# Kernel optimization log

Measured on AMD Instinct MI355X. Metric: run time of the kernel, lower is better.

The kernel has to match this reference:

```python
import jax, jax.numpy as jnp
import numpy as np

B, D, N = 2, 256, 8192   # batch, in_channels, sequence length
CI = 128                 # inter_channels
BN_EPS = 1e-5


def conv1x1(w, b, x):
    # w: (Cout, Cin), b: (Cout,), x: (B, Cin, N) -> (B, Cout, N)
    return jnp.einsum('oc,bcn->bon', w, x) + b[None, :, None]


def maxpool2(x):
    # MaxPool1d(kernel_size=2): (B, C, N) -> (B, C, N//2)
    b, c, n = x.shape
    return x.reshape(b, c, n // 2, 2).max(axis=-1)


def setup_inputs() -> dict:
    key = jax.random.key(0)
    ks = jax.random.split(key, 11)
    s_in = 1.0 / np.sqrt(D)
    s_ci = 1.0 / np.sqrt(CI)
    return {
        'f': jax.random.normal(ks[0], (B, D, N), dtype=jnp.float32),
        'g_w': jax.random.uniform(ks[1], (CI, D), jnp.float32, -s_in, s_in),
        'g_b': jax.random.uniform(ks[2], (CI,), jnp.float32, -s_in, s_in),
        'theta_w': jax.random.uniform(ks[3], (CI, D), jnp.float32, -s_in, s_in),
        'theta_b': jax.random.uniform(ks[4], (CI,), jnp.float32, -s_in, s_in),
        'phi_w': jax.random.uniform(ks[5], (CI, D), jnp.float32, -s_in, s_in),
        'phi_b': jax.random.uniform(ks[6], (CI,), jnp.float32, -s_in, s_in),
        'W_w': jax.random.uniform(ks[7], (D, CI), jnp.float32, -s_ci, s_ci),
        'W_b': jax.random.uniform(ks[8], (D,), jnp.float32, -s_ci, s_ci),
        'bn_gamma': jax.random.normal(ks[9], (D,), dtype=jnp.float32) * 0.1,
        'bn_beta': jax.random.normal(ks[10], (D,), dtype=jnp.float32) * 0.1,
    }


def reference(f, g_w, g_b, theta_w, theta_b, phi_w, phi_b, W_w, W_b, bn_gamma, bn_beta):
    # projections (1x1 convs); g and phi are sub-sampled by maxpool(2)
    g_f = maxpool2(conv1x1(g_w, g_b, f))          # (B, CI, N/2)
    theta_f = conv1x1(theta_w, theta_b, f)        # (B, CI, N)
    phi_f = maxpool2(conv1x1(phi_w, phi_b, f))    # (B, CI, N/2)

    # affinity: theta^T @ phi, softmax over keys (no scale, as in source)
    A = jnp.einsum('bcn,bcm->bnm', theta_f, phi_f)     # (B, N, N/2)
    A = jax.nn.softmax(A, axis=-1)
    y = jnp.einsum('bnm,bcm->bcn', A, g_f)             # (B, CI, N)

    # W: 1x1 conv + BatchNorm1d (training-mode batch stats), residual
    Wy = conv1x1(W_w, W_b, y)                          # (B, D, N)
    mean = Wy.mean(axis=(0, 2), keepdims=True)
    var = Wy.var(axis=(0, 2), keepdims=True)           # biased, like torch BN
    Wy = (Wy - mean) * jax.lax.rsqrt(var + BN_EPS)
    Wy = Wy * bn_gamma[None, :, None] + bn_beta[None, :, None]
    return Wy + f
```

## Files before the change

kernel.cpp:

```cpp
#include <hip/hip_runtime.h>
#include <hip/hip_bf16.h>
#include <math.h>

#define B_ 2
#define D_ 256
#define N_ 8192
#define CI_ 128
#define M_ 4096
#define BN_EPS_ 1e-5f
#define LOG2E_ 1.4426950408889634f

#define GLOBAL_AS __attribute__((address_space(1)))
#define LDS_AS __attribute__((address_space(3)))

#define OFF_WALL 0
#define OFF_THT  65536
#define OFF_PHT  (OFF_THT + 1048576)
#define OFF_GT   (OFF_PHT + 524288)
#define OFF_YP   (OFF_GT  + 524288)
#define OFF_ML   (OFF_YP  + 4194304)
#define OFF_MEAN (OFF_ML + 131072)
#define OFF_RSTD (OFF_MEAN + 256)

typedef __attribute__((ext_vector_type(8))) short bfrag;
typedef __attribute__((ext_vector_type(4))) float f4v;
typedef __attribute__((ext_vector_type(16))) float f16v;
typedef __attribute__((ext_vector_type(4))) short s4v;
typedef __attribute__((ext_vector_type(4))) unsigned u4v;

__device__ inline unsigned short bf16rne(float x) {
    unsigned u = __float_as_uint(x);
    u += 0x7fff + ((u >> 16) & 1);
    return (unsigned short)(u >> 16);
}

__device__ inline float exp2fast(float x) {
    float r;
    asm("v_exp_f32 %0, %1" : "=v"(r) : "v"(x));
    return r;
}

__global__ __launch_bounds__(256) void wconv_kernel(
    const float* __restrict__ gw, const float* __restrict__ tw, const float* __restrict__ pw,
    const float* __restrict__ Ww, short* __restrict__ wall)
{
    int idx = blockIdx.x * 256 + threadIdx.x;
    int which = idx >> 15;
    int rem = idx & 32767;
    const float* src = (which == 0) ? gw : (which == 1) ? tw : (which == 2) ? pw : Ww;
    float v = src[rem];
    if (which == 1) v *= LOG2E_;
    wall[idx] = (short)bf16rne(v);
}

__global__ __launch_bounds__(256, 2) void proj_kernel(
    const float* __restrict__ f, const short* __restrict__ wall,
    const float* __restrict__ tb, const float* __restrict__ gb, const float* __restrict__ pb,
    short* __restrict__ th_t, short* __restrict__ g_t, short* __restrict__ ph_t)
{
    __shared__ short sF[32 * 72];

    const int tid = threadIdx.x;
    const int wave = tid >> 6, lane = tid & 63;
    const int lq = lane & 15, quad = lane >> 4;
    const int b = blockIdx.y;
    const int n0 = blockIdx.x * 32;

    const float* fb = f + (size_t)b * D_ * N_;

    f4v acc[6][2];
#pragma unroll
    for (int ct = 0; ct < 6; ct++)
#pragma unroll
        for (int nf = 0; nf < 2; nf++) acc[ct][nf] = (f4v){0.f, 0.f, 0.f, 0.f};

    const int sn = tid & 31;
    const int sgrp = tid >> 5;

    for (int kc = 0; kc < D_; kc += 64) {
        __syncthreads();
#pragma unroll
        for (int jj = 0; jj < 4; jj++) {
            int dd = kc + sgrp * 8 + 2 * jj;
            float v0 = fb[(size_t)dd * N_ + n0 + sn];
            float v1 = fb[(size_t)(dd + 1) * N_ + n0 + sn];
            unsigned pk = (unsigned)bf16rne(v0) | ((unsigned)bf16rne(v1) << 16);
            *(unsigned*)&sF[sn * 72 + sgrp * 8 + 2 * jj] = pk;
        }
        __syncthreads();

        bfrag afr[6][2], bfr[2][2];
#pragma unroll
        for (int ks = 0; ks < 2; ks++) {
#pragma unroll
            for (int nf = 0; nf < 2; nf++)
                bfr[nf][ks] = *(const bfrag*)&sF[(nf * 16 + lq) * 72 + ks * 32 + quad * 8];
#pragma unroll
            for (int ct = 0; ct < 6; ct++)
                afr[ct][ks] = *(const bfrag*)&wall[(wave * 96 + ct * 16 + lq) * 256 + kc + ks * 32 + quad * 8];
        }
#pragma unroll
        for (int ks = 0; ks < 2; ks++)
#pragma unroll
            for (int ct = 0; ct < 6; ct++) {
                acc[ct][0] = __builtin_amdgcn_mfma_f32_16x16x32_bf16(afr[ct][ks], bfr[0][ks], acc[ct][0], 0, 0, 0);
                acc[ct][1] = __builtin_amdgcn_mfma_f32_16x16x32_bf16(afr[ct][ks], bfr[1][ks], acc[ct][1], 0, 0, 0);
            }
    }

#pragma unroll
    for (int ct = 0; ct < 6; ct++) {
        const int cf = wave * 6 + ct;
#pragma unroll
        for (int nf = 0; nf < 2; nf++) {
            f4v v = acc[ct][nf];
            const int n = n0 + nf * 16 + lq;
            if (cf < 8) {
                const int cb = cf * 16 + quad * 4;
                float pl[4];
#pragma unroll
                for (int r = 0; r < 4; r++) {
                    float o = __shfl_xor(v[r], 1);
                    pl[r] = fmaxf(v[r], o) + gb[cb + r];
                }
                if (!(lq & 1)) {
                    const int m = n >> 1;
#pragma unroll
                    for (int r = 0; r < 4; r++)
                        g_t[((size_t)b * CI_ + cb + r) * M_ + m] = (short)bf16rne(pl[r]);
                }
            } else if (cf < 16) {
                const int cb = (cf - 8) * 16 + quad * 4;
                s4v o;
#pragma unroll
                for (int r = 0; r < 4; r++) o[r] = (short)bf16rne(v[r] + tb[cb + r] * LOG2E_);
                *(s4v*)&th_t[((size_t)b * N_ + n) * CI_ + cb] = o;
            } else {
                const int cb = (cf - 16) * 16 + quad * 4;
                float pl[4];
#pragma unroll
                for (int r = 0; r < 4; r++) {
                    float o = __shfl_xor(v[r], 1);
                    pl[r] = fmaxf(v[r], o) + pb[cb + r];
                }
                if (!(lq & 1)) {
                    const int m = n >> 1;
                    s4v o;
#pragma unroll
                    for (int r = 0; r < 4; r++) o[r] = (short)bf16rne(pl[r]);
                    *(s4v*)&ph_t[((size_t)b * M_ + m) * CI_ + cb] = o;
                }
            }
        }
    }
}

__global__ __launch_bounds__(256, 2) void attn_kernel(
    const short* __restrict__ th_p, const short* __restrict__ ph_p,
    const short* __restrict__ g_p, short* __restrict__ yp, float* __restrict__ ml)
{
    __shared__ short sPh[2][64 * 128];
    __shared__ short sG [2][128 * 72];

    const int tid = threadIdx.x;
    const int wave = tid >> 6, lane = tid & 63;
    const int l = lane & 31, h = lane >> 5;

    const int bid = blockIdx.x;
    const int b = bid & 1;
    const int split = (bid >> 1) & 3;
    const int q0 = (bid >> 3) * 128;
    const int qg = q0 + wave * 32 + l;

    const short* thr = th_p + ((size_t)b * N_ + qg) * CI_;
    bfrag tf[8];
#pragma unroll
    for (int s = 0; s < 8; s++)
        tf[s] = *(const bfrag*)&thr[s * 16 + h * 8];

    f16v yacc[4];
#pragma unroll
    for (int ct = 0; ct < 4; ct++)
#pragma unroll
        for (int r = 0; r < 16; r++) yacc[ct][r] = 0.f;
    float mI = -INFINITY, lI = 0.f;

    const short* phg = ph_p + (size_t)b * M_ * CI_;
    const short* gg  = g_p + (size_t)b * CI_ * M_;

    const int k0 = split * 1024;
    const int xm = l & 15;

    const int prow = (lane >> 4);
    const int pslot = lane & 15;

    const int i0 = (wave < 2) ? wave * 5 : 10 + (wave - 2) * 4;
    const int nIss = (wave < 2) ? 5 : 4;
    int gsrc[5];
#pragma unroll
    for (int p = 0; p < 5; p++) {
        const int t = (i0 + p) * 64 + lane;
        gsrc[p] = (t / 9) * M_ + (t % 9) * 8;
    }

#define STAGE_DMA(BUF, KC)                                                                  \
    do {                                                                                    \
        _Pragma("unroll")                                                                   \
        for (int p = 0; p < 4; p++) {                                                       \
            const int rp = wave * 16 + p * 4 + prow;                     \
            const int cg = pslot ^ (p * 4 + prow);                   \
            __builtin_amdgcn_global_load_lds(                                               \
                (const GLOBAL_AS void*)(phg + (size_t)((KC) + rp) * 128 + cg * 8),          \
                (LDS_AS void*)(&sPh[BUF][(wave * 16 + p * 4) * 128]), 16, 0, 0);            \
        }                                                                                   \
        _Pragma("unroll")                                                                   \
        for (int p = 0; p < 5; p++) {                                                       \
            if (p < nIss)                                                                   \
                __builtin_amdgcn_global_load_lds(                                           \
                    (const GLOBAL_AS void*)(gg + gsrc[p] + (KC)),                           \
                    (LDS_AS void*)(&sG[BUF][(i0 + p) * 512]), 16, 0, 0);                    \
        }                                                                                   \
    } while (0)

    STAGE_DMA(0, k0);

    int cur = 0;
    for (int kc = k0; kc < k0 + 1024; kc += 64) {
        __syncthreads();
        const bool nxt = (kc + 64 < k0 + 1024);
        if (nxt) {
            STAGE_DMA(cur ^ 1, kc + 64);
            __builtin_amdgcn_sched_barrier(0);
        }

        f16v sv[2];
        __builtin_amdgcn_s_setprio(1);
#pragma unroll
        for (int kt = 0; kt < 2; kt++) {
            f16v a;
#pragma unroll
            for (int r = 0; r < 16; r++) a[r] = 0.f;
#pragma unroll
            for (int s = 0; s < 8; s++) {
                bfrag pa = *(const bfrag*)&sPh[cur][(kt * 32 + l) * 128 + (((s << 1) | h) ^ xm) * 8];
                a = __builtin_amdgcn_mfma_f32_32x32x16_bf16(pa, tf[s], a, 0, 0, 0);
            }
            sv[kt] = a;
        }
        __builtin_amdgcn_s_setprio(0);

        float mx = fmaxf(sv[0][0], sv[1][0]);
#pragma unroll
        for (int r = 1; r < 16; r++) mx = fmaxf(mx, fmaxf(sv[0][r], sv[1][r]));
        mx = fmaxf(mx, __shfl_xor(mx, 32));

        if (__any(mx > mI + 8.f)) {
            float mnew = fmaxf(mI, mx);
            float al = exp2fast(mI - mnew);
            lI *= al;
#pragma unroll
            for (int ct = 0; ct < 4; ct++)
#pragma unroll
                for (int r = 0; r < 16; r++) yacc[ct][r] *= al;
            mI = mnew;
        }

        float ps = 0.f;
        unsigned pw[16];
#pragma unroll
        for (int kt = 0; kt < 2; kt++)
#pragma unroll
            for (int i = 0; i < 8; i++) {
                const int r = 2 * i;
                float p0 = exp2fast(sv[kt][r] - mI);
                float p1 = exp2fast(sv[kt][r + 1] - mI);
                ps += p0 + p1;
                unsigned pk;
                asm("v_cvt_pk_bf16_f32 %0, %1, %2" : "=v"(pk) : "v"(p0), "v"(p1));
                pw[kt * 8 + (i >> 1) * 2 + (i & 1)] = pk;
            }
        ps += __shfl_xor(ps, 32);
        lI += ps;

        bfrag pf[4];
#pragma unroll
        for (int s = 0; s < 4; s++) {
            const int kt = s >> 1;
            const int iA = kt * 8 + ((2 * s) & 3) * 2;
            const int iB = kt * 8 + ((2 * s + 1) & 3) * 2;
            unsigned A0 = pw[iA], A1 = pw[iA + 1];
            unsigned B0 = pw[iB], B1 = pw[iB + 1];
            unsigned O0 = h ? B0 : A0;
            unsigned O1 = h ? B1 : A1;
            unsigned Xs0 = h ? A0 : B0;
            unsigned Xs1 = h ? A1 : B1;
            unsigned X0 = (unsigned)__shfl_xor((int)Xs0, 32);
            unsigned X1 = (unsigned)__shfl_xor((int)Xs1, 32);
            u4v t;
            t.x = h ? X0 : O0;
            t.y = h ? X1 : O1;
            t.z = h ? O0 : X0;
            t.w = h ? O1 : X1;
            pf[s] = __builtin_bit_cast(bfrag, t);
        }

        __builtin_amdgcn_s_setprio(1);
#pragma unroll
        for (int ct = 0; ct < 4; ct++)
#pragma unroll
            for (int s = 0; s < 4; s++) {
                bfrag ga = *(const bfrag*)&sG[cur][(ct * 32 + l) * 72 + s * 16 + h * 8];
                yacc[ct] = __builtin_amdgcn_mfma_f32_32x32x16_bf16(ga, pf[s], yacc[ct], 0, 0, 0);
            }
        __builtin_amdgcn_s_setprio(0);

        cur ^= 1;
    }
#undef STAGE_DMA

    short* yb = yp + (((size_t)split * B_ + b) * N_) * CI_;
#pragma unroll
    for (int ct = 0; ct < 4; ct++)
#pragma unroll
        for (int rq = 0; rq < 4; rq++) {
            const int c0 = ct * 32 + 8 * rq + 4 * h;
            s4v o;
#pragma unroll
            for (int j = 0; j < 4; j++) o[j] = (short)bf16rne(yacc[ct][rq * 4 + j]);
            *(s4v*)&yb[(size_t)qg * CI_ + c0] = o;
        }
    if (h == 0) {
        float* mlb = ml + ((split * B_ + b) * 2) * N_;
        mlb[qg] = mI;
        mlb[N_ + qg] = lI;
    }
}

__global__ __launch_bounds__(256) void wy_merge_kernel(
    const short* __restrict__ yp, const float* __restrict__ ml,
    const short* __restrict__ wall2, const float* __restrict__ Wb,
    float* __restrict__ out)
{
    const int tid = threadIdx.x;
    const int wave = tid >> 6, lane = tid & 63;
    const int l = lane & 31, h = lane >> 5;
    const int b = blockIdx.y;
    const int n = blockIdx.x * 32 + l;

    float m[4], lv[4];
#pragma unroll
    for (int sp = 0; sp < 4; sp++) {
        const float* mlb = ml + ((sp * B_ + b) * 2) * N_;
        m[sp] = mlb[n];
        lv[sp] = mlb[N_ + n];
    }
    float mmax = fmaxf(fmaxf(m[0], m[1]), fmaxf(m[2], m[3]));
    float e[4], den = 0.f;
#pragma unroll
    for (int sp = 0; sp < 4; sp++) { e[sp] = exp2fast(m[sp] - mmax); den += lv[sp] * e[sp]; }
    float inv = 1.0f / den;
#pragma unroll
    for (int sp = 0; sp < 4; sp++) e[sp] *= inv;

    bfrag by[8];
#pragma unroll
    for (int s = 0; s < 8; s++) {
        float a[8];
#pragma unroll
        for (int j = 0; j < 8; j++) a[j] = 0.f;
#pragma unroll
        for (int sp = 0; sp < 4; sp++) {
            bfrag yv = *(const bfrag*)&yp[(((size_t)sp * B_ + b) * N_ + n) * CI_ + s * 16 + h * 8];
            u4v u = __builtin_bit_cast(u4v, yv);
#pragma unroll
            for (int p = 0; p < 4; p++) {
                a[2 * p]     = fmaf(e[sp], __uint_as_float(u[p] << 16), a[2 * p]);
                a[2 * p + 1] = fmaf(e[sp], __uint_as_float(u[p] & 0xffff0000u), a[2 * p + 1]);
            }
        }
        u4v pk;
#pragma unroll
        for (int p = 0; p < 4; p++) {
            unsigned r;
            asm("v_cvt_pk_bf16_f32 %0, %1, %2" : "=v"(r) : "v"(a[2 * p]), "v"(a[2 * p + 1]));
            pk[p] = r;
        }
        by[s] = __builtin_bit_cast(bfrag, pk);
    }

    f16v acc[2];
#pragma unroll
    for (int rt = 0; rt < 2; rt++)
#pragma unroll
        for (int r = 0; r < 16; r++) acc[rt][r] = 0.f;

#pragma unroll
    for (int s = 0; s < 8; s++)
#pragma unroll
        for (int rt = 0; rt < 2; rt++) {
            bfrag aw = *(const bfrag*)&wall2[((wave * 2 + rt) * 32 + l) * 128 + s * 16 + h * 8];
            acc[rt] = __builtin_amdgcn_mfma_f32_32x32x16_bf16(aw, by[s], acc[rt], 0, 0, 0);
        }

#pragma unroll
    for (int rt = 0; rt < 2; rt++)
#pragma unroll
        for (int r = 0; r < 16; r++) {
            const int d = (wave * 2 + rt) * 32 + (r & 3) + 8 * (r >> 2) + 4 * h;
            out[((size_t)b * D_ + d) * N_ + n] = acc[rt][r] + Wb[d];
        }
}

__global__ __launch_bounds__(256) void stats_kernel(
    const float* __restrict__ wy, float* __restrict__ mean, float* __restrict__ rstd)
{
    __shared__ float ssum[256], ssq[256];
    int d = blockIdx.x;
    int tid = threadIdx.x;
    float s = 0.f, sq = 0.f;
    for (int b = 0; b < B_; b++) {
        const float4* p = (const float4*)(wy + (size_t)b * D_ * N_ + (size_t)d * N_);
        for (int i = tid; i < N_ / 4; i += 256) {
            float4 v = p[i];
            s += v.x + v.y + v.z + v.w;
            sq = fmaf(v.x, v.x, sq);
            sq = fmaf(v.y, v.y, sq);
            sq = fmaf(v.z, v.z, sq);
            sq = fmaf(v.w, v.w, sq);
        }
    }
    ssum[tid] = s; ssq[tid] = sq;
    __syncthreads();
    for (int st = 128; st > 0; st >>= 1) {
        if (tid < st) { ssum[tid] += ssum[tid + st]; ssq[tid] += ssq[tid + st]; }
        __syncthreads();
    }
    if (tid == 0) {
        float inv = 1.0f / (float)(B_ * N_);
        float mn = ssum[0] * inv;
        float var = ssq[0] * inv - mn * mn;
        mean[d] = mn;
        rstd[d] = rsqrtf(var + BN_EPS_);
    }
}

__global__ __launch_bounds__(256) void bn_res_kernel(
    float* __restrict__ out, const float* __restrict__ f,
    const float* __restrict__ mean, const float* __restrict__ rstd,
    const float* __restrict__ gamma, const float* __restrict__ beta)
{
    int i = blockIdx.x * 256 + threadIdx.x;
    size_t e = (size_t)i * 4;
    int d = (int)((e >> 13) & 255);
    float4 wy = ((const float4*)out)[i];
    float4 ff = ((const float4*)f)[i];
    float sc = rstd[d] * gamma[d];
    float mn = mean[d];
    float bt = beta[d];
    float4 r;
    r.x = (wy.x - mn) * sc + bt + ff.x;
    r.y = (wy.y - mn) * sc + bt + ff.y;
    r.z = (wy.z - mn) * sc + bt + ff.z;
    r.w = (wy.w - mn) * sc + bt + ff.w;
    ((float4*)out)[i] = r;
}

extern "C" void kernel_launch(void* const* d_in, const int* in_sizes, int n_in,
                              void* d_out, int out_size, void* d_ws, size_t ws_size,
                              hipStream_t stream)
{
    const float* f   = (const float*)d_in[0];
    const float* g_w = (const float*)d_in[1];
    const float* g_b = (const float*)d_in[2];
    const float* t_w = (const float*)d_in[3];
    const float* t_b = (const float*)d_in[4];
    const float* p_w = (const float*)d_in[5];
    const float* p_b = (const float*)d_in[6];
    const float* W_w = (const float*)d_in[7];
    const float* W_b = (const float*)d_in[8];
    const float* gam = (const float*)d_in[9];
    const float* bet = (const float*)d_in[10];
    float* out = (float*)d_out;
    float* ws = (float*)d_ws;

    short* wall  = (short*)(ws + OFF_WALL);
    short* wall2 = wall + 3 * 32768;
    short* th_t = (short*)(ws + OFF_THT);
    short* ph_t = (short*)(ws + OFF_PHT);
    short* g_t  = (short*)(ws + OFF_GT);
    short* ypart = (short*)(ws + OFF_YP);
    float* mlp = ws + OFF_ML;
    float* mnp = ws + OFF_MEAN;
    float* rsp = ws + OFF_RSTD;

    wconv_kernel<<<512, 256, 0, stream>>>(g_w, t_w, p_w, W_w, wall);
    proj_kernel<<<dim3(N_ / 32, B_), 256, 0, stream>>>(f, wall, t_b, g_b, p_b,
                                                       th_t, g_t, ph_t);
    attn_kernel<<<512, 256, 0, stream>>>(th_t, ph_t, g_t, ypart, mlp);
    wy_merge_kernel<<<dim3(N_ / 32, B_), 256, 0, stream>>>(ypart, mlp, wall2, W_b, out);
    stats_kernel<<<D_, 256, 0, stream>>>(out, mnp, rsp);
    bn_res_kernel<<<(B_ * D_ * N_ / 4) / 256, 256, 0, stream>>>(out, f, mnp, rsp, gam, bet);
}
```

Baseline: 180.0 us.

## Single-buffer phi tile, raise occupancy, and add 8-way key split

The phi LDS tile goes from double- to single-buffered. Its next-chunk load is now issued after a mid-iteration barrier, once the S=QK MFMAs have consumed the current tile. Launch bounds rise to 3 blocks per CU, and with a large enough workspace the key dimension is split 8 ways (1024 blocks), templating the merge kernel on the split count. The max reduction becomes a tree and the exp/pack loop is fused with the cross-half shuffle. Together these aim for more occupancy and parallelism, at the cost of an extra barrier per iteration, more partial-output traffic, and possible register spilling at 3 blocks/CU.

```diff
diff --git a/kernel.cpp b/kernel.cpp
--- a/kernel.cpp
+++ b/kernel.cpp
@@ -18,9 +18,6 @@
 #define OFF_PHT  (OFF_THT + 1048576)
 #define OFF_GT   (OFF_PHT + 524288)
 #define OFF_YP   (OFF_GT  + 524288)
-#define OFF_ML   (OFF_YP  + 4194304)
-#define OFF_MEAN (OFF_ML + 131072)
-#define OFF_RSTD (OFF_MEAN + 256)
 
 typedef __attribute__((ext_vector_type(8))) short bfrag;
 typedef __attribute__((ext_vector_type(4))) float f4v;
@@ -155,11 +152,13 @@
     }
 }
 
-__global__ __launch_bounds__(256, 2) void attn_kernel(
+template<int NS>
+__global__ __launch_bounds__(256, 3) void attn_kernel(
     const short* __restrict__ th_p, const short* __restrict__ ph_p,
     const short* __restrict__ g_p, short* __restrict__ yp, float* __restrict__ ml)
 {
-    __shared__ short sPh[2][64 * 128];
+    constexpr int SK = M_ / NS;
+    __shared__ short sPh[64 * 128];
     __shared__ short sG [2][128 * 72];
 
     const int tid = threadIdx.x;
@@ -167,9 +166,10 @@
     const int l = lane & 31, h = lane >> 5;
 
     const int bid = blockIdx.x;
-    const int b = bid & 1;
-    const int split = (bid >> 1) & 3;
-    const int q0 = (bid >> 3) * 128;
+    const int pair = bid & (2 * NS - 1);
+    const int b = pair & 1;
+    const int split = pair >> 1;
+    const int q0 = (bid / (2 * NS)) * 128;
     const int qg = q0 + wave * 32 + l;
 
     const short* thr = th_p + ((size_t)b * N_ + qg) * CI_;
@@ -188,7 +188,7 @@
     const short* phg = ph_p + (size_t)b * M_ * CI_;
     const short* gg  = g_p + (size_t)b * CI_ * M_;
 
-    const int k0 = split * 1024;
+    const int k0 = split * SK;
     const int xm = l & 15;
 
     const int prow = (lane >> 4);
@@ -203,7 +203,7 @@
         gsrc[p] = (t / 9) * M_ + (t % 9) * 8;
     }
 
-#define STAGE_DMA(BUF, KC)                                                                  \
+#define STAGE_PHI(KC)                                                                       \
     do {                                                                                    \
         _Pragma("unroll")                                                                   \
         for (int p = 0; p < 4; p++) {                                                       \
@@ -211,8 +211,11 @@
             const int cg = pslot ^ (p * 4 + prow);                   \
             __builtin_amdgcn_global_load_lds(                                               \
                 (const GLOBAL_AS void*)(phg + (size_t)((KC) + rp) * 128 + cg * 8),          \
-                (LDS_AS void*)(&sPh[BUF][(wave * 16 + p * 4) * 128]), 16, 0, 0);            \
+                (LDS_AS void*)(&sPh[(wave * 16 + p * 4) * 128]), 16, 0, 0);                 \
         }                                                                                   \
+    } while (0)
+#define STAGE_G(BUF, KC)                                                                    \
+    do {                                                                                    \
         _Pragma("unroll")                                                                   \
         for (int p = 0; p < 5; p++) {                                                       \
             if (p < nIss)                                                                   \
@@ -222,14 +225,15 @@
         }                                                                                   \
     } while (0)
 
-    STAGE_DMA(0, k0);
+    STAGE_PHI(k0);
+    STAGE_G(0, k0);
 
     int cur = 0;
-    for (int kc = k0; kc < k0 + 1024; kc += 64) {
+    for (int kc = k0; kc < k0 + SK; kc += 64) {
         __syncthreads();
-        const bool nxt = (kc + 64 < k0 + 1024);
+        const bool nxt = (kc + 64 < k0 + SK);
         if (nxt) {
-            STAGE_DMA(cur ^ 1, kc + 64);
+            STAGE_G(cur ^ 1, kc + 64);
             __builtin_amdgcn_sched_barrier(0);
         }
 
@@ -242,17 +246,31 @@
             for (int r = 0; r < 16; r++) a[r] = 0.f;
 #pragma unroll
             for (int s = 0; s < 8; s++) {
-                bfrag pa = *(const bfrag*)&sPh[cur][(kt * 32 + l) * 128 + (((s << 1) | h) ^ xm) * 8];
+                bfrag pa = *(const bfrag*)&sPh[(kt * 32 + l) * 128 + (((s << 1) | h) ^ xm) * 8];
                 a = __builtin_amdgcn_mfma_f32_32x32x16_bf16(pa, tf[s], a, 0, 0, 0);
             }
             sv[kt] = a;
         }
         __builtin_amdgcn_s_setprio(0);
 
-        float mx = fmaxf(sv[0][0], sv[1][0]);
-#pragma unroll
-        for (int r = 1; r < 16; r++) mx = fmaxf(mx, fmaxf(sv[0][r], sv[1][r]));
-        mx = fmaxf(mx, __shfl_xor(mx, 32));
+        __builtin_amdgcn_sched_barrier(0);
+        __builtin_amdgcn_s_barrier();
+        if (nxt) {
+            STAGE_PHI(kc + 64);
+            __builtin_amdgcn_sched_barrier(0);
+        }
+
+        float mx;
+        {
+            float t[16];
+#pragma unroll
+            for (int r = 0; r < 16; r++) t[r] = fmaxf(sv[0][r], sv[1][r]);
+#pragma unroll
+            for (int st = 8; st > 0; st >>= 1)
+#pragma unroll
+                for (int r = 0; r < st; r++) t[r] = fmaxf(t[r], t[r + st]);
+            mx = fmaxf(t[0], __shfl_xor(t[0], 32));
+        }
 
         if (__any(mx > mI + 8.f)) {
             float mnew = fmaxf(mI, mx);
@@ -266,34 +284,24 @@
         }
 
         float ps = 0.f;
-        unsigned pw[16];
-#pragma unroll
-        for (int kt = 0; kt < 2; kt++)
-#pragma unroll
-            for (int i = 0; i < 8; i++) {
-                const int r = 2 * i;
-                float p0 = exp2fast(sv[kt][r] - mI);
-                float p1 = exp2fast(sv[kt][r + 1] - mI);
-                ps += p0 + p1;
-                unsigned pk;
-                asm("v_cvt_pk_bf16_f32 %0, %1, %2" : "=v"(pk) : "v"(p0), "v"(p1));
-                pw[kt * 8 + (i >> 1) * 2 + (i & 1)] = pk;
-            }
-        ps += __shfl_xor(ps, 32);
-        lI += ps;
-
         bfrag pf[4];
 #pragma unroll
         for (int s = 0; s < 4; s++) {
             const int kt = s >> 1;
-            const int iA = kt * 8 + ((2 * s) & 3) * 2;
-            const int iB = kt * 8 + ((2 * s + 1) & 3) * 2;
-            unsigned A0 = pw[iA], A1 = pw[iA + 1];
-            unsigned B0 = pw[iB], B1 = pw[iB + 1];
-            unsigned O0 = h ? B0 : A0;
-            unsigned O1 = h ? B1 : A1;
-            unsigned Xs0 = h ? A0 : B0;
-            unsigned Xs1 = h ? A1 : B1;
+            const int rb = (s & 1) * 8;
+            float p[8];
+#pragma unroll
+            for (int j = 0; j < 8; j++) p[j] = exp2fast(sv[kt][rb + j] - mI);
+            ps += ((p[0] + p[1]) + (p[2] + p[3])) + ((p[4] + p[5]) + (p[6] + p[7]));
+            unsigned w0, w1, w2, w3;
+            asm("v_cvt_pk_bf16_f32 %0, %1, %2" : "=v"(w0) : "v"(p[0]), "v"(p[1]));
+            asm("v_cvt_pk_bf16_f32 %0, %1, %2" : "=v"(w1) : "v"(p[2]), "v"(p[3]));
+            asm("v_cvt_pk_bf16_f32 %0, %1, %2" : "=v"(w2) : "v"(p[4]), "v"(p[5]));
+            asm("v_cvt_pk_bf16_f32 %0, %1, %2" : "=v"(w3) : "v"(p[6]), "v"(p[7]));
+            unsigned O0 = h ? w2 : w0;
+            unsigned O1 = h ? w3 : w1;
+            unsigned Xs0 = h ? w0 : w2;
+            unsigned Xs1 = h ? w1 : w3;
             unsigned X0 = (unsigned)__shfl_xor((int)Xs0, 32);
             unsigned X1 = (unsigned)__shfl_xor((int)Xs1, 32);
             u4v t;
@@ -303,6 +311,8 @@
             t.w = h ? O1 : X1;
             pf[s] = __builtin_bit_cast(bfrag, t);
         }
+        ps += __shfl_xor(ps, 32);
+        lI += ps;
 
         __builtin_amdgcn_s_setprio(1);
 #pragma unroll
@@ -316,7 +326,8 @@
 
         cur ^= 1;
     }
-#undef STAGE_DMA
+#undef STAGE_PHI
+#undef STAGE_G
 
     short* yb = yp + (((size_t)split * B_ + b) * N_) * CI_;
 #pragma unroll
@@ -336,6 +347,7 @@
     }
 }
 
+template<int NS>
 __global__ __launch_bounds__(256) void wy_merge_kernel(
     const short* __restrict__ yp, const float* __restrict__ ml,
     const short* __restrict__ wall2, const float* __restrict__ Wb,
@@ -347,20 +359,22 @@
     const int b = blockIdx.y;
     const int n = blockIdx.x * 32 + l;
 
-    float m[4], lv[4];
-#pragma unroll
-    for (int sp = 0; sp < 4; sp++) {
+    float m[NS], lv[NS];
+#pragma unroll
+    for (int sp = 0; sp < NS; sp++) {
         const float* mlb = ml + ((sp * B_ + b) * 2) * N_;
         m[sp] = mlb[n];
         lv[sp] = mlb[N_ + n];
     }
-    float mmax = fmaxf(fmaxf(m[0], m[1]), fmaxf(m[2], m[3]));
-    float e[4], den = 0.f;
-#pragma unroll
-    for (int sp = 0; sp < 4; sp++) { e[sp] = exp2fast(m[sp] - mmax); den += lv[sp] * e[sp]; }
+    float mmax = m[0];
+#pragma unroll
+    for (int sp = 1; sp < NS; sp++) mmax = fmaxf(mmax, m[sp]);
+    float e[NS], den = 0.f;
+#pragma unroll
+    for (int sp = 0; sp < NS; sp++) { e[sp] = exp2fast(m[sp] - mmax); den += lv[sp] * e[sp]; }
     float inv = 1.0f / den;
 #pragma unroll
-    for (int sp = 0; sp < 4; sp++) e[sp] *= inv;
+    for (int sp = 0; sp < NS; sp++) e[sp] *= inv;
 
     bfrag by[8];
 #pragma unroll
@@ -369,7 +383,7 @@
 #pragma unroll
         for (int j = 0; j < 8; j++) a[j] = 0.f;
 #pragma unroll
-        for (int sp = 0; sp < 4; sp++) {
+        for (int sp = 0; sp < NS; sp++) {
             bfrag yv = *(const bfrag*)&yp[(((size_t)sp * B_ + b) * N_ + n) * CI_ + s * 16 + h * 8];
             u4v u = __builtin_bit_cast(u4v, yv);
 #pragma unroll
@@ -483,21 +497,29 @@
     float* out = (float*)d_out;
     float* ws = (float*)d_ws;
 
+    const size_t need8 = ((size_t)OFF_YP + 8u * 1048576u + 8u * 32768u + 512u) * 4u;
+    const int ns = (ws_size >= need8) ? 8 : 4;
+
     short* wall  = (short*)(ws + OFF_WALL);
     short* wall2 = wall + 3 * 32768;
     short* th_t = (short*)(ws + OFF_THT);
     short* ph_t = (short*)(ws + OFF_PHT);
     short* g_t  = (short*)(ws + OFF_GT);
     short* ypart = (short*)(ws + OFF_YP);
-    float* mlp = ws + OFF_ML;
-    float* mnp = ws + OFF_MEAN;
-    float* rsp = ws + OFF_RSTD;
+    float* mlp = ws + OFF_YP + (size_t)ns * 1048576u;
+    float* mnp = mlp + (size_t)ns * 32768u;
+    float* rsp = mnp + 256;
 
     wconv_kernel<<<512, 256, 0, stream>>>(g_w, t_w, p_w, W_w, wall);
     proj_kernel<<<dim3(N_ / 32, B_), 256, 0, stream>>>(f, wall, t_b, g_b, p_b,
                                                        th_t, g_t, ph_t);
-    attn_kernel<<<512, 256, 0, stream>>>(th_t, ph_t, g_t, ypart, mlp);
-    wy_merge_kernel<<<dim3(N_ / 32, B_), 256, 0, stream>>>(ypart, mlp, wall2, W_b, out);
+    if (ns == 8) {
+        attn_kernel<8><<<1024, 256, 0, stream>>>(th_t, ph_t, g_t, ypart, mlp);
+        wy_merge_kernel<8><<<dim3(N_ / 32, B_), 256, 0, stream>>>(ypart, mlp, wall2, W_b, out);
+    } else {
+        attn_kernel<4><<<512, 256, 0, stream>>>(th_t, ph_t, g_t, ypart, mlp);
+        wy_merge_kernel<4><<<dim3(N_ / 32, B_), 256, 0, stream>>>(ypart, mlp, wall2, W_b, out);
+    }
     stats_kernel<<<D_, 256, 0, stream>>>(out, mnp, rsp);
     bn_res_kernel<<<(B_ * D_ * N_ / 4) / 256, 256, 0, stream>>>(out, f, mnp, rsp, gam, bet);
 }
```

Result: slower. 208.2 us (+15.7%).
